# Kernel optimization log

Hardware: AMD Instinct MI355X
Metric: run time of the kernel (lower is better)

Reference implementation:

```python
import jax, jax.numpy as jnp
import numpy as np

VOCAB = 64
H = 64
B = 128
L = 2048


def setup_inputs() -> dict:
    key = jax.random.key(0)
    ks = jax.random.split(key, 14)
    s = 0.02
    return {
        "x": jax.random.randint(ks[0], (B, L), 0, VOCAB),
        "embed": jax.random.normal(ks[1], (VOCAB, H), jnp.float32) * s,
        "w1": jax.random.normal(ks[2], (2 * H, H), jnp.float32) * s,
        "b1": jnp.zeros((2 * H,), jnp.float32),
        "w2": jax.random.normal(ks[3], (H, 2 * H), jnp.float32) * s,
        "b2": jnp.zeros((H,), jnp.float32),
        "ln_g": jnp.ones((H,), jnp.float32),
        "ln_b": jnp.zeros((H,), jnp.float32),
        "Wk": jax.random.normal(ks[4], (H, H), jnp.float32) * s,
        "Wv": jax.random.normal(ks[5], (H, H), jnp.float32) * s,
        "Wq": jax.random.normal(ks[6], (H, H), jnp.float32) * s,
        "Wout": jax.random.normal(ks[7], (VOCAB, H), jnp.float32) * s,
        "bout": jnp.zeros((VOCAB,), jnp.float32),
    }


def _encoder(x, embed, w1, b1, w2, b2, ln_g, ln_b):
    h0 = embed[x]  # [B,L,H]
    ff = jnp.maximum(h0 @ w1.T + b1, 0.0) @ w2.T + b2
    z = h0 + ff
    mu = z.mean(-1, keepdims=True)
    var = ((z - mu) ** 2).mean(-1, keepdims=True)
    return (z - mu) * jax.lax.rsqrt(var + 1e-5) * ln_g + ln_b


def reference(x, embed, w1, b1, w2, b2, ln_g, ln_b, Wk, Wv, Wq, Wout, bout):
    h = _encoder(x, embed, w1, b1, w2, b2, ln_g, ln_b)  # [B,L,H]
    K = h @ Wk.T
    K = K / jnp.maximum(jnp.linalg.norm(K, axis=-1, keepdims=True), 1e-12)  # F.normalize
    V = h @ Wv.T
    b, l, hd = h.shape

    def step(M, kv):
        k, v = kv  # [B,H], [B,H]
        pred = jnp.einsum('bij,bj->bi', M, k)  # M @ k
        M = M + (v - pred)[:, :, None] * k[:, None, :]  # delta-rule outer update
        return M, None

    M0 = jnp.zeros((b, hd, hd), h.dtype)
    M, _ = jax.lax.scan(step, M0, (K.transpose(1, 0, 2), V.transpose(1, 0, 2)))

    q = h[:, -1] @ Wq.T  # [B,H]
    slots = M.transpose(0, 2, 1)  # M^T per batch: [B,H,H]
    scores = jnp.einsum('bij,bj->bi', slots, q) / jnp.sqrt(jnp.asarray(hd, h.dtype))
    attn = jax.nn.softmax(scores, axis=-1)  # [B,H]
    ctx = jnp.einsum('bi,bij->bj', attn, slots)  # [B,H]
    return jnp.maximum(ctx, 0.0) @ Wout.T + bout  # [B,VOCAB]
```

## Files before the change

kernel.cpp:

```cpp
#include <hip/hip_runtime.h>
#include <hip/hip_bf16.h>

#define VOCAB 64
#define H 64
#define NB 128
#define SL 2048

__global__ __launch_bounds__(64) void k_tables(
    const float* __restrict__ embed, const float* __restrict__ w1, const float* __restrict__ b1,
    const float* __restrict__ w2, const float* __restrict__ b2,
    const float* __restrict__ ln_g, const float* __restrict__ ln_b,
    const float* __restrict__ Wk, const float* __restrict__ Wv, const float* __restrict__ Wq,
    float* __restrict__ Ktab, float* __restrict__ Vtab, float* __restrict__ qtab)
{
  const int t = blockIdx.x;
  const int i = threadIdx.x;
  __shared__ float h0s[H];
  __shared__ float ff1s[2 * H];
  __shared__ float hs[H];

  h0s[i] = embed[t * H + i];
  __syncthreads();

  const float4* w1v = (const float4*)w1;
  float a0 = b1[i], a1 = b1[i + H];
#pragma unroll
  for (int j4 = 0; j4 < 16; ++j4) {
    const float4 hv = *(const float4*)&h0s[j4 * 4];
    const float4 wa = w1v[i * 16 + j4];
    const float4 wb = w1v[(i + H) * 16 + j4];
    a0 = fmaf(wa.x, hv.x, fmaf(wa.y, hv.y, fmaf(wa.z, hv.z, fmaf(wa.w, hv.w, a0))));
    a1 = fmaf(wb.x, hv.x, fmaf(wb.y, hv.y, fmaf(wb.z, hv.z, fmaf(wb.w, hv.w, a1))));
  }
  ff1s[i] = fmaxf(a0, 0.f);
  ff1s[i + H] = fmaxf(a1, 0.f);
  __syncthreads();

  const float4* w2v = (const float4*)w2;
  float z = h0s[i] + b2[i];
#pragma unroll
  for (int o4 = 0; o4 < 32; ++o4) {
    const float4 fv = *(const float4*)&ff1s[o4 * 4];
    const float4 wv = w2v[i * 32 + o4];
    z = fmaf(wv.x, fv.x, fmaf(wv.y, fv.y, fmaf(wv.z, fv.z, fmaf(wv.w, fv.w, z))));
  }

  float s = z;
#pragma unroll
  for (int m = 1; m < 64; m <<= 1) s += __shfl_xor(s, m);
  const float mu = s * (1.f / 64.f);
  const float d = z - mu;
  float s2 = d * d;
#pragma unroll
  for (int m = 1; m < 64; m <<= 1) s2 += __shfl_xor(s2, m);
  const float var = s2 * (1.f / 64.f);
  const float hv2 = d * rsqrtf(var + 1e-5f) * ln_g[i] + ln_b[i];
  hs[i] = hv2;
  __syncthreads();

  const float4* wkv = (const float4*)Wk;
  const float4* wvv = (const float4*)Wv;
  const float4* wqv = (const float4*)Wq;
  float kk = 0.f, vv = 0.f, qq = 0.f;
#pragma unroll
  for (int j4 = 0; j4 < 16; ++j4) {
    const float4 hj = *(const float4*)&hs[j4 * 4];
    const float4 ak = wkv[i * 16 + j4];
    const float4 av = wvv[i * 16 + j4];
    const float4 aq = wqv[i * 16 + j4];
    kk = fmaf(ak.x, hj.x, fmaf(ak.y, hj.y, fmaf(ak.z, hj.z, fmaf(ak.w, hj.w, kk))));
    vv = fmaf(av.x, hj.x, fmaf(av.y, hj.y, fmaf(av.z, hj.z, fmaf(av.w, hj.w, vv))));
    qq = fmaf(aq.x, hj.x, fmaf(aq.y, hj.y, fmaf(aq.z, hj.z, fmaf(aq.w, hj.w, qq))));
  }
  float n2 = kk * kk;
#pragma unroll
  for (int m = 1; m < 64; m <<= 1) n2 += __shfl_xor(n2, m);
  const float inv = 1.f / fmaxf(sqrtf(n2), 1e-12f);
  Ktab[t * H + i] = kk * inv;
  Vtab[t * H + i] = vv;
  qtab[t * H + i] = qq;
}

__device__ __forceinline__ float rdl(float v, int sl) {
  return __int_as_float(__builtin_amdgcn_readlane(__float_as_int(v), sl));
}

__global__ __launch_bounds__(512) void k_scan(
    const int* __restrict__ x, const float* __restrict__ Ktab, const float* __restrict__ Vtab,
    float* __restrict__ Mout)
{
  const int bb = blockIdx.x >> 1;
  const int half = blockIdx.x & 1;
  const int tid = threadIdx.x;
  const int lane = tid & 63;
  const int wave = tid >> 6;
  const int r0 = wave * 4;

  __shared__ float smem[16448];
  float* Ks  = smem;
  float* KTs = smem + 4096;
  float* GKs = smem + 8256;

#pragma unroll
  for (int u = 0; u < 2; ++u) {
    const int f4i = u * 512 + tid;
    const float4 kv = ((const float4*)Ktab)[f4i];
    ((float4*)Ks)[f4i] = kv;
    const int row = f4i >> 4, c4 = (f4i & 15) * 4;
    KTs[(c4 + 0) * 65 + row] = kv.x;
    KTs[(c4 + 1) * 65 + row] = kv.y;
    KTs[(c4 + 2) * 65 + row] = kv.z;
    KTs[(c4 + 3) * 65 + row] = kv.w;
  }
#pragma unroll
  for (int u = 0; u < 8; ++u) {
    const int idx = u * 512 + tid;
    GKs[idx * 2 + 1] = Ktab[idx];
  }
  __syncthreads();

  {
    const int abase = wave * 8;
#pragma unroll 1
    for (int ar = 0; ar < 8; ++ar) {
      const int a = abase + ar;
      float acc = 0.f;
#pragma unroll
      for (int i = 0; i < H; i += 4) {
        const float4 ka = *(const float4*)&Ks[a * 64 + i];
        acc = fmaf(ka.x, KTs[(i + 0) * 65 + lane], acc);
        acc = fmaf(ka.y, KTs[(i + 1) * 65 + lane], acc);
        acc = fmaf(ka.z, KTs[(i + 2) * 65 + lane], acc);
        acc = fmaf(ka.w, KTs[(i + 3) * 65 + lane], acc);
      }
      GKs[(a * 64 + lane) * 2] = acc;
    }
  }
  __syncthreads();

  float Q[4], Mr[4];
#pragma unroll
  for (int j = 0; j < 4; ++j) {
    Q[j] = -Vtab[lane * H + half * 32 + r0 + j];
    Mr[j] = 0.f;
  }

  const int* __restrict__ xp = x + bb * SL;
  const int lane2 = lane * 2;

  float gA, kA, gB, kB, gC, kC, gD, kD;

#define PREF(G_, K_, a_)                                                   \
  {                                                                        \
    const float2 gk = *(const float2*)&GKs[(a_) * 128 + lane2];            \
    G_ = gk.x; K_ = gk.y;                                                  \
  }

#define STEP(G_, K_, a_)                                                   \
  {                                                                        \
    const float q0 = rdl(Q[0], a_);                                        \
    const float q1 = rdl(Q[1], a_);                                        \
    const float q2 = rdl(Q[2], a_);                                        \
    const float q3 = rdl(Q[3], a_);                                        \
    Q[0] = fmaf(-q0, G_, Q[0]);  Mr[0] = fmaf(-q0, K_, Mr[0]);             \
    Q[1] = fmaf(-q1, G_, Q[1]);  Mr[1] = fmaf(-q1, K_, Mr[1]);             \
    Q[2] = fmaf(-q2, G_, Q[2]);  Mr[2] = fmaf(-q2, K_, Mr[2]);             \
    Q[3] = fmaf(-q3, G_, Q[3]);  Mr[3] = fmaf(-q3, K_, Mr[3]);             \
  }

  int4 tg = *(const int4*)(xp);
  PREF(gA, kA, tg.x);
  PREF(gB, kB, tg.y);

#pragma unroll 1
  for (int n = 0; n < SL / 4; ++n) {
    const int offn = (n + 1 < SL / 4) ? (n + 1) * 4 : 0;
    const int4 tgN = *(const int4*)(xp + offn);
    PREF(gC, kC, tg.z);
    STEP(gA, kA, tg.x);
    PREF(gD, kD, tg.w);
    STEP(gB, kB, tg.y);
    PREF(gA, kA, tgN.x);
    STEP(gC, kC, tg.z);
    PREF(gB, kB, tgN.y);
    STEP(gD, kD, tg.w);
    tg = tgN;
  }
#undef PREF
#undef STEP

  float* mp = Mout + ((size_t)bb * H + half * 32 + r0) * H + lane;
#pragma unroll
  for (int j = 0; j < 4; ++j) mp[j * H] = Mr[j];
}

__global__ __launch_bounds__(64) void k_final(
    const int* __restrict__ x, const float* __restrict__ Mws, const float* __restrict__ qtab,
    const float* __restrict__ Wout, const float* __restrict__ bout, float* __restrict__ out)
{
  const int b = blockIdx.x;
  const int i = threadIdx.x;
  __shared__ float Ml[H * 65];
  __shared__ float qs[H];
  __shared__ float attns[H];
  __shared__ float rcs[H];

  const float* Mg = Mws + (size_t)b * H * H;
#pragma unroll
  for (int j4 = 0; j4 < H; j4 += 4) {
    const float4 v = *(const float4*)(Mg + i * H + j4);
    Ml[i * 65 + j4 + 0] = v.x;
    Ml[i * 65 + j4 + 1] = v.y;
    Ml[i * 65 + j4 + 2] = v.z;
    Ml[i * 65 + j4 + 3] = v.w;
  }
  const int tok = x[b * SL + (SL - 1)];
  qs[i] = qtab[tok * H + i];
  __syncthreads();

  float acc = 0.f;
#pragma unroll
  for (int j = 0; j < H; ++j) acc = fmaf(Ml[j * 65 + i], qs[j], acc);
  const float sc = acc * 0.125f;

  float mx = sc;
#pragma unroll
  for (int m = 1; m < 64; m <<= 1) mx = fmaxf(mx, __shfl_xor(mx, m));
  const float e = expf(sc - mx);
  float ssum = e;
#pragma unroll
  for (int m = 1; m < 64; m <<= 1) ssum += __shfl_xor(ssum, m);
  attns[i] = e / ssum;
  __syncthreads();

  float cx = 0.f;
#pragma unroll
  for (int jj = 0; jj < H; ++jj) cx = fmaf(attns[jj], Ml[i * 65 + jj], cx);
  rcs[i] = fmaxf(cx, 0.f);
  __syncthreads();

  float o = bout[i];
#pragma unroll
  for (int j = 0; j < H; ++j) o = fmaf(Wout[i * H + j], rcs[j], o);
  out[b * VOCAB + i] = o;
}

extern "C" void kernel_launch(void* const* d_in, const int* in_sizes, int n_in,
                              void* d_out, int out_size, void* d_ws, size_t ws_size,
                              hipStream_t stream) {
  const int*   x     = (const int*)d_in[0];
  const float* embed = (const float*)d_in[1];
  const float* w1    = (const float*)d_in[2];
  const float* b1    = (const float*)d_in[3];
  const float* w2    = (const float*)d_in[4];
  const float* b2    = (const float*)d_in[5];
  const float* ln_g  = (const float*)d_in[6];
  const float* ln_b  = (const float*)d_in[7];
  const float* Wk    = (const float*)d_in[8];
  const float* Wv    = (const float*)d_in[9];
  const float* Wq    = (const float*)d_in[10];
  const float* Wout  = (const float*)d_in[11];
  const float* bout  = (const float*)d_in[12];

  float* ws   = (float*)d_ws;
  float* Ktab = ws;
  float* Vtab = ws + 4096;
  float* qtab = ws + 8192;
  float* Mws  = ws + 12288;

  k_tables<<<dim3(VOCAB), dim3(H), 0, stream>>>(embed, w1, b1, w2, b2, ln_g, ln_b,
                                                Wk, Wv, Wq, Ktab, Vtab, qtab);
  k_scan<<<dim3(2 * NB), dim3(512), 0, stream>>>(x, Ktab, Vtab, Mws);
  k_final<<<dim3(NB), dim3(64), 0, stream>>>(x, Mws, qtab, Wout, bout, (float*)d_out);
}
```

Baseline: 212.8 us.

## Split scan rows across four blocks per batch and deepen token prefetch

```diff
diff --git a/kernel.cpp b/kernel.cpp
--- a/kernel.cpp
+++ b/kernel.cpp
@@ -85,16 +85,16 @@
   return __int_as_float(__builtin_amdgcn_readlane(__float_as_int(v), sl));
 }
 
-__global__ __launch_bounds__(512) void k_scan(
+__global__ __launch_bounds__(512, 4) void k_scan(
     const int* __restrict__ x, const float* __restrict__ Ktab, const float* __restrict__ Vtab,
     float* __restrict__ Mout)
 {
-  const int bb = blockIdx.x >> 1;
-  const int half = blockIdx.x & 1;
+  const int bb = blockIdx.x >> 2;
+  const int quarter = blockIdx.x & 3;
   const int tid = threadIdx.x;
   const int lane = tid & 63;
   const int wave = tid >> 6;
-  const int r0 = wave * 4;
+  const int grow = quarter * 16 + wave * 2;
 
   __shared__ float smem[16448];
   float* Ks  = smem;
@@ -138,12 +138,10 @@
   }
   __syncthreads();
 
-  float Q[4], Mr[4];
-#pragma unroll
-  for (int j = 0; j < 4; ++j) {
-    Q[j] = -Vtab[lane * H + half * 32 + r0 + j];
-    Mr[j] = 0.f;
-  }
+  float Q[2], Mr[2];
+  Q[0] = -Vtab[lane * H + grow + 0];
+  Q[1] = -Vtab[lane * H + grow + 1];
+  Mr[0] = 0.f; Mr[1] = 0.f;
 
   const int* __restrict__ xp = x + bb * SL;
   const int lane2 = lane * 2;
@@ -160,22 +158,19 @@
   {                                                                        \
     const float q0 = rdl(Q[0], a_);                                        \
     const float q1 = rdl(Q[1], a_);                                        \
-    const float q2 = rdl(Q[2], a_);                                        \
-    const float q3 = rdl(Q[3], a_);                                        \
     Q[0] = fmaf(-q0, G_, Q[0]);  Mr[0] = fmaf(-q0, K_, Mr[0]);             \
     Q[1] = fmaf(-q1, G_, Q[1]);  Mr[1] = fmaf(-q1, K_, Mr[1]);             \
-    Q[2] = fmaf(-q2, G_, Q[2]);  Mr[2] = fmaf(-q2, K_, Mr[2]);             \
-    Q[3] = fmaf(-q3, G_, Q[3]);  Mr[3] = fmaf(-q3, K_, Mr[3]);             \
-  }
-
-  int4 tg = *(const int4*)(xp);
+  }
+
+  int4 tg  = *(const int4*)(xp);
+  int4 tgN = *(const int4*)(xp + 4);
   PREF(gA, kA, tg.x);
   PREF(gB, kB, tg.y);
 
 #pragma unroll 1
   for (int n = 0; n < SL / 4; ++n) {
-    const int offn = (n + 1 < SL / 4) ? (n + 1) * 4 : 0;
-    const int4 tgN = *(const int4*)(xp + offn);
+    const int offnn = (n + 2 < SL / 4) ? (n + 2) * 4 : 0;
+    const int4 tgNN = *(const int4*)(xp + offnn);
     PREF(gC, kC, tg.z);
     STEP(gA, kA, tg.x);
     PREF(gD, kD, tg.w);
@@ -184,14 +179,14 @@
     STEP(gC, kC, tg.z);
     PREF(gB, kB, tgN.y);
     STEP(gD, kD, tg.w);
-    tg = tgN;
+    tg = tgN; tgN = tgNN;
   }
 #undef PREF
 #undef STEP
 
-  float* mp = Mout + ((size_t)bb * H + half * 32 + r0) * H + lane;
-#pragma unroll
-  for (int j = 0; j < 4; ++j) mp[j * H] = Mr[j];
+  float* mp = Mout + ((size_t)bb * H + grow) * H + lane;
+  mp[0] = Mr[0];
+  mp[H] = Mr[1];
 }
 
 __global__ __launch_bounds__(64) void k_final(
@@ -270,6 +265,6 @@
 
   k_tables<<<dim3(VOCAB), dim3(H), 0, stream>>>(embed, w1, b1, w2, b2, ln_g, ln_b,
                                                 Wk, Wv, Wq, Ktab, Vtab, qtab);
-  k_scan<<<dim3(2 * NB), dim3(512), 0, stream>>>(x, Ktab, Vtab, Mws);
+  k_scan<<<dim3(4 * NB), dim3(512), 0, stream>>>(x, Ktab, Vtab, Mws);
   k_final<<<dim3(NB), dim3(64), 0, stream>>>(x, Mws, qtab, Wout, bout, (float*)d_out);
 }
```

Result: slower. 256.9 us (+20.7%).
